# Performance work log

Measured on AMD Instinct MI355X. Metric: run time of the kernel, lower is better.

Reference implementation:

```python
import jax, jax.numpy as jnp
import numpy as np

B, S, H = 1, 4096, 2048
NH, NKV, HD = 8, 4, 256
I = 8192
EPS = 1e-6
THETA = 10000.0
WINDOW = 4096  # hardcoded sliding window for even layer_idx
LAYER_IDX = 0


def rms_norm(x, w):
    v = jnp.mean(jnp.square(x), axis=-1, keepdims=True)
    return x * jax.lax.rsqrt(v + EPS) * w


def rotate_half(x):
    h = x.shape[-1] // 2
    return jnp.concatenate([-x[..., h:], x[..., :h]], axis=-1)


def apply_rope(q, k, positions):
    # q: [B,S,NH,HD], k: [B,S,NKV,HD], positions: [B,S]
    inv_freq = 1.0 / (THETA ** (jnp.arange(0, HD, 2, dtype=jnp.float32) / HD))
    freqs = positions.astype(jnp.float32)[..., None] * inv_freq  # [B,S,HD/2]
    emb = jnp.concatenate([freqs, freqs], axis=-1)               # [B,S,HD]
    cos = jnp.cos(emb)[:, :, None, :]
    sin = jnp.sin(emb)[:, :, None, :]
    q = q * cos + rotate_half(q) * sin
    k = k * cos + rotate_half(k) * sin
    return q, k


def forward(hidden_states, q_w, k_w, v_w, o_w, gate_w, up_w, down_w, ln1_w, ln2_w,
            attention_mask, position_ids):
    # ---- input RMSNorm + attention ----
    residual = hidden_states
    x = rms_norm(hidden_states, ln1_w)

    q = (x @ q_w).reshape(B, S, NH, HD)
    k = (x @ k_w).reshape(B, S, NKV, HD)
    v = (x @ v_w).reshape(B, S, NKV, HD)
    q, k = apply_rope(q, k, position_ids)

    # GQA: repeat kv heads to match query heads
    groups = NH // NKV
    k = jnp.repeat(k, groups, axis=2)  # [B,S,NH,HD]
    v = jnp.repeat(v, groups, axis=2)

    # masks: padding mask AND causal AND (even layer) local window of WINDOW
    row = jnp.arange(S)[:, None]
    col = jnp.arange(S)[None, :]
    causal = col <= row                                   # [S,S]
    combined = causal[None, None] & (attention_mask[:, None, None, :] > 0)
    if LAYER_IDX % 2 == 0:
        keep = ~(col <= row - WINDOW)                     # mask out keys older than WINDOW
        combined = combined & keep[None, None]
    neg = jnp.finfo(jnp.float32).min
    bias = jnp.where(combined, 0.0, neg).astype(jnp.float32)  # [B,1,S,S]

    scale = HD ** -0.5
    scores = jnp.einsum('bqhd,bkhd->bhqk', q, k) * scale + bias
    probs = jax.nn.softmax(scores, axis=-1)
    attn = jnp.einsum('bhqk,bkhd->bqhd', probs, v).reshape(B, S, NH * HD)
    attn_out = attn @ o_w

    hidden_states = residual + attn_out

    # ---- post-attention RMSNorm + gated-GeLU MLP ----
    residual = hidden_states
    x = rms_norm(hidden_states, ln2_w)
    mlp = (jax.nn.gelu(x @ gate_w, approximate=True) * (x @ up_w)) @ down_w
    return residual + mlp


def setup_inputs() -> dict:
    key = jax.random.key(0)
    ks = jax.random.split(key, 9)
    std = 0.02
    n = lambda k, shp: jax.random.normal(k, shp, dtype=jnp.float32) * std
    return {
        'hidden_states': jax.random.normal(ks[0], (B, S, H), dtype=jnp.float32),
        'q_w': n(ks[1], (H, NH * HD)),
        'k_w': n(ks[2], (H, NKV * HD)),
        'v_w': n(ks[3], (H, NKV * HD)),
        'o_w': n(ks[4], (NH * HD, H)),
        'gate_w': n(ks[5], (H, I)),
        'up_w': n(ks[6], (H, I)),
        'down_w': n(ks[7], (I, H)),
        'ln1_w': jnp.ones((H,), jnp.float32),
        'ln2_w': jnp.ones((H,), jnp.float32),
        'attention_mask': jnp.ones((B, S), jnp.int32),
        'position_ids': jnp.broadcast_to(jnp.arange(S, dtype=jnp.int32)[None, :], (B, S)),
    }


def reference(hidden_states, q_w, k_w, v_w, o_w, gate_w, up_w, down_w, ln1_w, ln2_w,
              attention_mask, position_ids):
    return forward(hidden_states, q_w, k_w, v_w, o_w, gate_w, up_w, down_w,
                   ln1_w, ln2_w, attention_mask, position_ids)
```

## Files before the change

kernel.cpp:

```cpp
#include <hip/hip_runtime.h>
#include <hip/hip_bf16.h>
#include <math.h>

#define S_LEN 4096
#define HID   2048
#define NHEADS 8
#define NKVH   4
#define HDIM   256
#define FFN    8192
#define WIN    4096
#define QKV_LD 4096

typedef __bf16 bf16_t;
typedef __bf16 bf16x4 __attribute__((ext_vector_type(4)));
typedef __bf16 bf16x8 __attribute__((ext_vector_type(8)));
typedef float  floatx4 __attribute__((ext_vector_type(4)));

#define WAITCNT_VM0   0x0f70
#define WAITCNT_VM8   0x0f78
#define WAITCNT_LGKM0 0xc07f

__device__ inline float waveReduceSum(float v) {
#pragma unroll
    for (int o = 32; o > 0; o >>= 1) v += __shfl_xor(v, o);
    return v;
}
__device__ inline float blockReduceSum(float v, float* sh) {
    int tid = threadIdx.x;
    v = waveReduceSum(v);
    if ((tid & 63) == 0) sh[tid >> 6] = v;
    __syncthreads();
    v = sh[0] + sh[1] + sh[2] + sh[3];
    __syncthreads();
    return v;
}

template <typename T>
__global__ __launch_bounds__(256) void transpose_bf16_kernel(const T* __restrict__ in,
                                                             bf16_t* __restrict__ out,
                                                             int ldin, int ldout) {
    __shared__ float tile[32][33];
    int tx = threadIdx.x & 31;
    int ty = threadIdx.x >> 5;
    int c0 = blockIdx.x * 32;
    int r0 = blockIdx.y * 32;
#pragma unroll
    for (int i = 0; i < 4; ++i)
        tile[ty + i * 8][tx] = (float)in[(long long)(r0 + ty + i * 8) * ldin + c0 + tx];
    __syncthreads();
#pragma unroll
    for (int i = 0; i < 4; ++i)
        out[(long long)(c0 + ty + i * 8) * ldout + r0 + tx] = (bf16_t)tile[tx][ty + i * 8];
}

__global__ __launch_bounds__(256) void rmsnorm_kernel(const float* __restrict__ x,
                                                      const float* __restrict__ w,
                                                      bf16_t* __restrict__ out) {
    __shared__ float sh[4];
    int row = blockIdx.x;
    const float* xr = x + (long long)row * HID;
    float v[8];
    float ss = 0.f;
#pragma unroll
    for (int i = 0; i < 8; ++i) {
        v[i] = xr[threadIdx.x + i * 256];
        ss += v[i] * v[i];
    }
    ss = blockReduceSum(ss, sh);
    float sc = rsqrtf(ss * (1.0f / HID) + 1e-6f);
#pragma unroll
    for (int i = 0; i < 8; ++i) {
        int c = threadIdx.x + i * 256;
        out[(long long)row * HID + c] = (bf16_t)(v[i] * sc * w[c]);
    }
}

__global__ __launch_bounds__(256) void rope_kernel(bf16_t* __restrict__ qkv,
                                                   const int* __restrict__ pos_ids) {
    int s = blockIdx.x;
    float p = (float)pos_ids[s];
    for (int t = threadIdx.x; t < (NHEADS + NKVH) * (HDIM / 2); t += 256) {
        int head = t >> 7;
        int i = t & 127;
        float inv = expf(-(2.0f * (float)i / (float)HDIM) * 9.210340371976184f);
        float f = p * inv;
        float sn, cs;
        sincosf(f, &sn, &cs);
        int col = (head < NHEADS) ? head * HDIM : HID + (head - NHEADS) * HDIM;
        bf16_t* base = qkv + (long long)s * QKV_LD + col;
        float a = (float)base[i];
        float b = (float)base[i + 128];
        base[i]       = (bf16_t)(a * cs - b * sn);
        base[i + 128] = (bf16_t)(b * cs + a * sn);
    }
}

__global__ __launch_bounds__(256) void flash_attn_kernel(const bf16_t* __restrict__ qkv,
                                                         const bf16_t* __restrict__ vTg,
                                                         bf16_t* __restrict__ op0,
                                                         bf16_t* __restrict__ op1,
                                                         float* __restrict__ mlb,
                                                         const int* __restrict__ amask) {
    __shared__ bf16_t sK[64 * 256];
    __shared__ bf16_t sV[256 * 64];
    __shared__ bf16_t sPb[4 * 16 * 72];

    const int h = blockIdx.y;
    const int kh = blockIdx.z;
    const int tid = threadIdx.x;
    const int lane = tid & 63;
    const int w = tid >> 6;
    const int tl = lane & 15;
    const int quad = lane >> 4;

    const bf16_t* Qh = qkv + h * HDIM;
    const bf16_t* Kh = qkv + HID + (h >> 1) * HDIM;
    const bf16_t* Vh = vTg + (long long)(h >> 1) * HDIM * S_LEN;
    bf16_t* Op = kh ? op1 : op0;
    bf16_t* sP = sPb + w * (16 * 72);

#pragma unroll 1
    for (int half = 0; half < 2; ++half) {
        const int qi = half ? (63 - blockIdx.x) : blockIdx.x;
        const int qr0 = qi * 64;
        const int ntiles = qi + 1;
        const int mid = ntiles >> 1;
        const int t0 = kh ? mid : 0;
        const int t1 = kh ? ntiles : mid;
        const int irow = qr0 + w * 16 + tl;

        const bf16_t* qrow = Qh + (long long)irow * QKV_LD;
        bf16x8 qf[8];
#pragma unroll
        for (int ks = 0; ks < 8; ++ks)
            qf[ks] = *(const bf16x8*)(qrow + (ks * 4 + quad) * 8);

        floatx4 oacc[16] = {};
        float m_i = -3e38f, l_i = 0.f;

        bf16x8 stK[8], stV[8];
        auto load_tile = [&](int kt) {
#pragma unroll
            for (int it = 0; it < 8; ++it) {
                int s = it * 256 + tid;
                {
                    int m = s >> 5, sg = s & 31, g = sg ^ (m & 7);
                    stK[it] = *(const bf16x8*)(Kh + (long long)(kt + m) * QKV_LD + g * 8);
                }
                {
                    int m = s >> 3, sg = s & 7, g = sg ^ (m & 7);
                    stV[it] = *(const bf16x8*)(Vh + (long long)m * S_LEN + kt + g * 8);
                }
            }
        };

        if (t0 < t1) load_tile(t0 * 64);

#pragma unroll 1
        for (int t = t0; t < t1; ++t) {
            const int kt = t * 64;
#pragma unroll
            for (int it = 0; it < 8; ++it) {
                int s = it * 256 + tid;
                *(bf16x8*)(sK + s * 8) = stK[it];
                *(bf16x8*)(sV + s * 8) = stV[it];
            }
            __syncthreads();

            if (t + 1 < t1) load_tile((t + 1) * 64);
            __builtin_amdgcn_sched_barrier(0);

            floatx4 sacc[4] = {};
            __builtin_amdgcn_s_setprio(1);
#pragma unroll
            for (int ks = 0; ks < 8; ++ks) {
                bf16x8 kf[4];
#pragma unroll
                for (int ni = 0; ni < 4; ++ni) {
                    int row = ni * 16 + tl;
                    int ph = (ks * 4 + quad) ^ (row & 7);
                    kf[ni] = *(const bf16x8*)(sK + row * 256 + ph * 8);
                }
#pragma unroll
                for (int ni = 0; ni < 4; ++ni)
                    sacc[ni] = __builtin_amdgcn_mfma_f32_16x16x32_bf16(kf[ni], qf[ks], sacc[ni], 0, 0, 0);
            }
            __builtin_amdgcn_s_setprio(0);

            float sv[4][4];
            float mx = -3e38f;
#pragma unroll
            for (int ni = 0; ni < 4; ++ni) {
                int4 am = *(const int4*)(amask + kt + ni * 16 + quad * 4);
#pragma unroll
                for (int r = 0; r < 4; ++r) {
                    int j = kt + ni * 16 + quad * 4 + r;
                    int amr = (r == 0) ? am.x : (r == 1) ? am.y : (r == 2) ? am.z : am.w;
                    bool valid = (j <= irow) && (j > irow - WIN) && (amr > 0);
                    float x = valid ? sacc[ni][r] * 0.0625f : -3e38f;
                    sv[ni][r] = x;
                    mx = fmaxf(mx, x);
                }
            }
            mx = fmaxf(mx, __shfl_xor(mx, 16));
            mx = fmaxf(mx, __shfl_xor(mx, 32));
            bool noresc = __all(mx <= m_i + 8.0f);
            float mnew = noresc ? m_i : fmaxf(m_i, mx);
            float rs = 0.f;
#pragma unroll
            for (int ni = 0; ni < 4; ++ni) {
                bf16x4 pk;
#pragma unroll
                for (int r = 0; r < 4; ++r) {
                    float p = (sv[ni][r] > -1e37f) ? __expf(sv[ni][r] - mnew) : 0.f;
                    rs += p;
                    pk[r] = (bf16_t)p;
                }
                *(bf16x4*)(sP + tl * 72 + ni * 16 + quad * 4) = pk;
            }
            rs += __shfl_xor(rs, 16);
            rs += __shfl_xor(rs, 32);
            if (noresc) {
                l_i += rs;
            } else {
                float alpha = __expf(m_i - mnew);
                l_i = l_i * alpha + rs;
                m_i = mnew;
                floatx4 av;
#pragma unroll
                for (int r = 0; r < 4; ++r) av[r] = __shfl(alpha, quad * 4 + r);
#pragma unroll
                for (int dt = 0; dt < 16; ++dt) oacc[dt] *= av;
            }

            __builtin_amdgcn_s_setprio(1);
#pragma unroll
            for (int k2 = 0; k2 < 2; ++k2) {
                bf16x8 pf = *(const bf16x8*)(sP + tl * 72 + k2 * 32 + quad * 8);
#pragma unroll
                for (int dt = 0; dt < 16; ++dt) {
                    int d = dt * 16 + tl;
                    int ph = (k2 * 4 + quad) ^ (d & 7);
                    bf16x8 vf = *(const bf16x8*)(sV + d * 64 + ph * 8);
                    oacc[dt] = __builtin_amdgcn_mfma_f32_16x16x32_bf16(pf, vf, oacc[dt], 0, 0, 0);
                }
            }
            __builtin_amdgcn_s_setprio(0);
            __syncthreads();
        }

        floatx4 inv;
#pragma unroll
        for (int r = 0; r < 4; ++r) {
            float lv = __shfl(l_i, quad * 4 + r);
            inv[r] = (lv > 0.f) ? 1.0f / lv : 0.f;
        }
#pragma unroll
        for (int dt = 0; dt < 16; ++dt) {
#pragma unroll
            for (int r = 0; r < 4; ++r) {
                long long row = qr0 + w * 16 + quad * 4 + r;
                Op[row * HID + h * HDIM + dt * 16 + tl] = (bf16_t)(oacc[dt][r] * inv[r]);
            }
        }
        if (quad == 0) {
            long long mi = ((long long)(kh * NHEADS + h) * S_LEN + qr0 + w * 16 + tl) * 2;
            mlb[mi] = m_i;
            mlb[mi + 1] = l_i;
        }
    }
}

__global__ __launch_bounds__(256) void combine_kernel(bf16_t* __restrict__ op0,
                                                      const bf16_t* __restrict__ op1,
                                                      const float* __restrict__ mlb) {
    int h = blockIdx.x;
    int row = blockIdx.y;
    int d = threadIdx.x;
    long long m0i = ((long long)h * S_LEN + row) * 2;
    long long m1i = ((long long)(NHEADS + h) * S_LEN + row) * 2;
    float m0 = mlb[m0i], l0 = mlb[m0i + 1];
    float m1 = mlb[m1i], l1 = mlb[m1i + 1];
    float M = fmaxf(m0, m1);
    float w0 = (l0 > 0.f) ? l0 * __expf(m0 - M) : 0.f;
    float w1 = (l1 > 0.f) ? l1 * __expf(m1 - M) : 0.f;
    float inv = 1.0f / (w0 + w1);
    long long idx = (long long)row * HID + h * HDIM + d;
    float v = (w0 * (float)op0[idx] + w1 * (float)op1[idx]) * inv;
    op0[idx] = (bf16_t)v;
}

template <int MODE>
__global__ __launch_bounds__(256) void gemm_kernel(const bf16_t* __restrict__ A, int lda,
                                                   const bf16_t* __restrict__ Bt, int ldb,
                                                   void* __restrict__ Cv, int ldc,
                                                   const void* __restrict__ aux, int K) {
    __shared__ bf16_t smem[2][2 * 128 * 64];

    const int tid = threadIdx.x;
    const int n0 = blockIdx.x * 128;
    const int m0 = blockIdx.y * 128;

    const int lane = tid & 63;
    const int wid = tid >> 6;
    const int wm = (wid >> 1) * 64;
    const int wn = (wid & 1) * 64;
    const int tl = lane & 15;
    const int quad = lane >> 4;

    floatx4 acc[4][4] = {};

    auto stage = [&](int buf, int k0) {
        bf16_t* sA = smem[buf];
        bf16_t* sB = smem[buf] + 128 * 64;
#pragma unroll
        for (int it = 0; it < 4; ++it) {
            int s = it * 256 + tid;
            int m = s >> 3;
            int sg = s & 7;
            int g = sg ^ (m & 7);
            const bf16_t* ga = A + (long long)(m0 + m) * lda + k0 + g * 8;
            __builtin_amdgcn_global_load_lds((const __attribute__((address_space(1))) void*)ga,
                                             (__attribute__((address_space(3))) void*)(sA + s * 8),
                                             16, 0, 0);
            const bf16_t* gb = Bt + (long long)(n0 + m) * ldb + k0 + g * 8;
            __builtin_amdgcn_global_load_lds((const __attribute__((address_space(1))) void*)gb,
                                             (__attribute__((address_space(3))) void*)(sB + s * 8),
                                             16, 0, 0);
        }
    };

    stage(0, 0);
    int cur = 0;

    for (int k0 = 0; k0 < K; k0 += 64) {
        if (k0 + 64 < K) {
            stage(cur ^ 1, k0 + 64);
            __builtin_amdgcn_s_waitcnt(WAITCNT_VM8);
        } else {
            __builtin_amdgcn_s_waitcnt(WAITCNT_VM0);
        }
        __builtin_amdgcn_s_barrier();
        __builtin_amdgcn_sched_barrier(0);

        const bf16_t* sA = smem[cur];
        const bf16_t* sB = smem[cur] + 128 * 64;
#pragma unroll
        for (int kk = 0; kk < 2; ++kk) {
            bf16x8 af[4], bfr[4];
#pragma unroll
            for (int mi = 0; mi < 4; ++mi) {
                int m = wm + mi * 16 + tl;
                int sg = (kk * 4 + quad) ^ (m & 7);
                af[mi] = *(const bf16x8*)(sA + m * 64 + sg * 8);
            }
#pragma unroll
            for (int ni = 0; ni < 4; ++ni) {
                int n = wn + ni * 16 + tl;
                int sg = (kk * 4 + quad) ^ (n & 7);
                bfr[ni] = *(const bf16x8*)(sB + n * 64 + sg * 8);
            }
#pragma unroll
            for (int mi = 0; mi < 4; ++mi)
#pragma unroll
                for (int ni = 0; ni < 4; ++ni)
                    acc[mi][ni] = __builtin_amdgcn_mfma_f32_16x16x32_bf16(af[mi], bfr[ni], acc[mi][ni], 0, 0, 0);
        }

        __builtin_amdgcn_s_waitcnt(WAITCNT_LGKM0);
        __builtin_amdgcn_sched_barrier(0);
        __builtin_amdgcn_s_barrier();
        cur ^= 1;
    }

#pragma unroll
    for (int mi = 0; mi < 4; ++mi) {
#pragma unroll
        for (int ni = 0; ni < 4; ++ni) {
#pragma unroll
            for (int r = 0; r < 4; ++r) {
                int gr = m0 + wm + mi * 16 + quad * 4 + r;
                int gc = n0 + wn + ni * 16 + tl;
                long long idx = (long long)gr * ldc + gc;
                float v = acc[mi][ni][r];
                if (MODE == 0) {
                    ((bf16_t*)Cv)[idx] = (bf16_t)v;
                } else if (MODE == 1) {
                    ((float*)Cv)[idx] = ((const float*)aux)[idx] + v;
                } else {
                    float g = (float)((const bf16_t*)aux)[idx];
                    float t = 0.7978845608028654f * (g + 0.044715f * g * g * g);
                    float ge = 0.5f * g * (1.0f + tanhf(t));
                    ((bf16_t*)Cv)[idx] = (bf16_t)(ge * v);
                }
            }
        }
    }
}

extern "C" void kernel_launch(void* const* d_in, const int* in_sizes, int n_in,
                              void* d_out, int out_size, void* d_ws, size_t ws_size,
                              hipStream_t stream) {
    const float* hidden = (const float*)d_in[0];
    const float* q_w    = (const float*)d_in[1];
    const float* k_w    = (const float*)d_in[2];
    const float* v_w    = (const float*)d_in[3];
    const float* o_w    = (const float*)d_in[4];
    const float* gate_w = (const float*)d_in[5];
    const float* up_w   = (const float*)d_in[6];
    const float* down_w = (const float*)d_in[7];
    const float* ln1_w  = (const float*)d_in[8];
    const float* ln2_w  = (const float*)d_in[9];
    const int* amask    = (const int*)d_in[10];
    const int* pos_ids  = (const int*)d_in[11];
    float* out = (float*)d_out;

    const size_t MB = 1ull << 20;
    char* ws = (char*)d_ws;
    bf16_t* wqT = (bf16_t*)(ws + 0 * MB);
    bf16_t* wkT = (bf16_t*)(ws + 8 * MB);
    bf16_t* wvT = (bf16_t*)(ws + 12 * MB);
    bf16_t* woT = (bf16_t*)(ws + 16 * MB);
    bf16_t* wgT = (bf16_t*)(ws + 24 * MB);
    bf16_t* wuT = (bf16_t*)(ws + 56 * MB);
    bf16_t* wdT = (bf16_t*)(ws + 88 * MB);
    bf16_t* xb    = (bf16_t*)(ws + 120 * MB);
    bf16_t* qkvb  = (bf16_t*)(ws + 136 * MB);
    bf16_t* vT    = (bf16_t*)(ws + 168 * MB);
    bf16_t* op0   = (bf16_t*)(ws + 120 * MB);
    bf16_t* op1   = (bf16_t*)(ws + 176 * MB);
    float*  mlb   = (float*) (ws + 192 * MB);
    bf16_t* attnb = (bf16_t*)(ws + 120 * MB);
    bf16_t* xb2   = (bf16_t*)(ws + 120 * MB);
    bf16_t* gateb = (bf16_t*)(ws + 136 * MB);
    (void)ws_size; (void)in_sizes; (void)n_in; (void)out_size;

    dim3 blk(256);

    transpose_bf16_kernel<float><<<dim3(64, 64), blk, 0, stream>>>(q_w, wqT, 2048, 2048);
    transpose_bf16_kernel<float><<<dim3(32, 64), blk, 0, stream>>>(k_w, wkT, 1024, 2048);
    transpose_bf16_kernel<float><<<dim3(32, 64), blk, 0, stream>>>(v_w, wvT, 1024, 2048);
    transpose_bf16_kernel<float><<<dim3(64, 64), blk, 0, stream>>>(o_w, woT, 2048, 2048);
    transpose_bf16_kernel<float><<<dim3(256, 64), blk, 0, stream>>>(gate_w, wgT, 8192, 2048);
    transpose_bf16_kernel<float><<<dim3(256, 64), blk, 0, stream>>>(up_w, wuT, 8192, 2048);
    transpose_bf16_kernel<float><<<dim3(64, 256), blk, 0, stream>>>(down_w, wdT, 2048, 8192);

    rmsnorm_kernel<<<dim3(S_LEN), blk, 0, stream>>>(hidden, ln1_w, xb);

    gemm_kernel<0><<<dim3(32, 32), blk, 0, stream>>>(xb, HID, wqT, HID, qkvb, QKV_LD, nullptr, HID);

    rope_kernel<<<dim3(S_LEN), blk, 0, stream>>>(qkvb, pos_ids);

    transpose_bf16_kernel<bf16_t><<<dim3(32, 128), blk, 0, stream>>>(qkvb + 3072, vT, QKV_LD, S_LEN);

    flash_attn_kernel<<<dim3(32, NHEADS, 2), blk, 0, stream>>>(qkvb, vT, op0, op1, mlb, amask);
    combine_kernel<<<dim3(NHEADS, S_LEN), blk, 0, stream>>>(op0, op1, mlb);

    gemm_kernel<1><<<dim3(16, 32), blk, 0, stream>>>(attnb, 2048, woT, 2048, out, 2048, hidden, 2048);

    rmsnorm_kernel<<<dim3(S_LEN), blk, 0, stream>>>(out, ln2_w, xb2);

    gemm_kernel<0><<<dim3(64, 32), blk, 0, stream>>>(xb2, HID, wgT, HID, gateb, FFN, nullptr, HID);
    gemm_kernel<2><<<dim3(64, 32), blk, 0, stream>>>(xb2, HID, wuT, HID, gateb, FFN, gateb, HID);
    gemm_kernel<1><<<dim3(16, 32), blk, 0, stream>>>(gateb, FFN, wdT, FFN, out, 2048, out, FFN);
}
```

Baseline: 1.152 ms.

## Split attention KV range four ways with 32-key tiles and higher occupancy

```diff
diff --git a/kernel.cpp b/kernel.cpp
--- a/kernel.cpp
+++ b/kernel.cpp
@@ -10,6 +10,7 @@
 #define FFN    8192
 #define WIN    4096
 #define QKV_LD 4096
+#define KVBLK  32
 
 typedef __bf16 bf16_t;
 typedef __bf16 bf16x4 __attribute__((ext_vector_type(4)));
@@ -95,15 +96,17 @@
     }
 }
 
-__global__ __launch_bounds__(256) void flash_attn_kernel(const bf16_t* __restrict__ qkv,
-                                                         const bf16_t* __restrict__ vTg,
-                                                         bf16_t* __restrict__ op0,
-                                                         bf16_t* __restrict__ op1,
-                                                         float* __restrict__ mlb,
-                                                         const int* __restrict__ amask) {
-    __shared__ bf16_t sK[64 * 256];
-    __shared__ bf16_t sV[256 * 64];
-    __shared__ bf16_t sPb[4 * 16 * 72];
+__global__ __launch_bounds__(256, 3) void flash_attn_kernel(const bf16_t* __restrict__ qkv,
+                                                            const bf16_t* __restrict__ vTg,
+                                                            bf16_t* __restrict__ op0,
+                                                            bf16_t* __restrict__ op1,
+                                                            bf16_t* __restrict__ op2,
+                                                            bf16_t* __restrict__ op3,
+                                                            float* __restrict__ mlb,
+                                                            const int* __restrict__ amask) {
+    __shared__ bf16_t sK[KVBLK * 256];
+    __shared__ bf16_t sV[256 * KVBLK];
+    __shared__ bf16_t sPb[4 * 16 * 40];
 
     const int h = blockIdx.y;
     const int kh = blockIdx.z;
@@ -116,17 +119,18 @@
     const bf16_t* Qh = qkv + h * HDIM;
     const bf16_t* Kh = qkv + HID + (h >> 1) * HDIM;
     const bf16_t* Vh = vTg + (long long)(h >> 1) * HDIM * S_LEN;
-    bf16_t* Op = kh ? op1 : op0;
-    bf16_t* sP = sPb + w * (16 * 72);
+    bf16_t* Op = (kh == 0) ? op0 : (kh == 1) ? op1 : (kh == 2) ? op2 : op3;
+    bf16_t* sP = sPb + w * (16 * 40);
 
 #pragma unroll 1
     for (int half = 0; half < 2; ++half) {
         const int qi = half ? (63 - blockIdx.x) : blockIdx.x;
         const int qr0 = qi * 64;
-        const int ntiles = qi + 1;
-        const int mid = ntiles >> 1;
-        const int t0 = kh ? mid : 0;
-        const int t1 = kh ? ntiles : mid;
+        const int ntiles = 2 * qi + 2;
+        const int q4 = ntiles >> 2;
+        const int r4 = ntiles & 3;
+        const int t0 = kh * q4 + ((kh < r4) ? kh : r4);
+        const int t1 = t0 + q4 + ((kh < r4) ? 1 : 0);
         const int irow = qr0 + w * 16 + tl;
 
         const bf16_t* qrow = Qh + (long long)irow * QKV_LD;
@@ -138,59 +142,59 @@
         floatx4 oacc[16] = {};
         float m_i = -3e38f, l_i = 0.f;
 
-        bf16x8 stK[8], stV[8];
+        bf16x8 stK[4], stV[4];
         auto load_tile = [&](int kt) {
 #pragma unroll
-            for (int it = 0; it < 8; ++it) {
+            for (int it = 0; it < 4; ++it) {
                 int s = it * 256 + tid;
                 {
                     int m = s >> 5, sg = s & 31, g = sg ^ (m & 7);
                     stK[it] = *(const bf16x8*)(Kh + (long long)(kt + m) * QKV_LD + g * 8);
                 }
                 {
-                    int m = s >> 3, sg = s & 7, g = sg ^ (m & 7);
+                    int m = s >> 2, sg = s & 3, g = sg ^ (m & 3);
                     stV[it] = *(const bf16x8*)(Vh + (long long)m * S_LEN + kt + g * 8);
                 }
             }
         };
 
-        if (t0 < t1) load_tile(t0 * 64);
+        if (t0 < t1) load_tile(t0 * KVBLK);
 
 #pragma unroll 1
         for (int t = t0; t < t1; ++t) {
-            const int kt = t * 64;
-#pragma unroll
-            for (int it = 0; it < 8; ++it) {
+            const int kt = t * KVBLK;
+#pragma unroll
+            for (int it = 0; it < 4; ++it) {
                 int s = it * 256 + tid;
                 *(bf16x8*)(sK + s * 8) = stK[it];
                 *(bf16x8*)(sV + s * 8) = stV[it];
             }
             __syncthreads();
 
-            if (t + 1 < t1) load_tile((t + 1) * 64);
+            if (t + 1 < t1) load_tile((t + 1) * KVBLK);
             __builtin_amdgcn_sched_barrier(0);
 
-            floatx4 sacc[4] = {};
+            floatx4 sacc[2] = {};
             __builtin_amdgcn_s_setprio(1);
 #pragma unroll
             for (int ks = 0; ks < 8; ++ks) {
-                bf16x8 kf[4];
-#pragma unroll
-                for (int ni = 0; ni < 4; ++ni) {
+                bf16x8 kf[2];
+#pragma unroll
+                for (int ni = 0; ni < 2; ++ni) {
                     int row = ni * 16 + tl;
                     int ph = (ks * 4 + quad) ^ (row & 7);
                     kf[ni] = *(const bf16x8*)(sK + row * 256 + ph * 8);
                 }
 #pragma unroll
-                for (int ni = 0; ni < 4; ++ni)
+                for (int ni = 0; ni < 2; ++ni)
                     sacc[ni] = __builtin_amdgcn_mfma_f32_16x16x32_bf16(kf[ni], qf[ks], sacc[ni], 0, 0, 0);
             }
             __builtin_amdgcn_s_setprio(0);
 
-            float sv[4][4];
+            float sv[2][4];
             float mx = -3e38f;
 #pragma unroll
-            for (int ni = 0; ni < 4; ++ni) {
+            for (int ni = 0; ni < 2; ++ni) {
                 int4 am = *(const int4*)(amask + kt + ni * 16 + quad * 4);
 #pragma unroll
                 for (int r = 0; r < 4; ++r) {
@@ -208,7 +212,7 @@
             float mnew = noresc ? m_i : fmaxf(m_i, mx);
             float rs = 0.f;
 #pragma unroll
-            for (int ni = 0; ni < 4; ++ni) {
+            for (int ni = 0; ni < 2; ++ni) {
                 bf16x4 pk;
 #pragma unroll
                 for (int r = 0; r < 4; ++r) {
@@ -216,7 +220,7 @@
                     rs += p;
                     pk[r] = (bf16_t)p;
                 }
-                *(bf16x4*)(sP + tl * 72 + ni * 16 + quad * 4) = pk;
+                *(bf16x4*)(sP + tl * 40 + ni * 16 + quad * 4) = pk;
             }
             rs += __shfl_xor(rs, 16);
             rs += __shfl_xor(rs, 32);
@@ -234,14 +238,13 @@
             }
 
             __builtin_amdgcn_s_setprio(1);
-#pragma unroll
-            for (int k2 = 0; k2 < 2; ++k2) {
-                bf16x8 pf = *(const bf16x8*)(sP + tl * 72 + k2 * 32 + quad * 8);
+            {
+                bf16x8 pf = *(const bf16x8*)(sP + tl * 40 + quad * 8);
 #pragma unroll
                 for (int dt = 0; dt < 16; ++dt) {
                     int d = dt * 16 + tl;
-                    int ph = (k2 * 4 + quad) ^ (d & 7);
-                    bf16x8 vf = *(const bf16x8*)(sV + d * 64 + ph * 8);
+                    int ph = quad ^ (d & 3);
+                    bf16x8 vf = *(const bf16x8*)(sV + d * KVBLK + ph * 8);
                     oacc[dt] = __builtin_amdgcn_mfma_f32_16x16x32_bf16(pf, vf, oacc[dt], 0, 0, 0);
                 }
             }
@@ -273,20 +276,31 @@
 
 __global__ __launch_bounds__(256) void combine_kernel(bf16_t* __restrict__ op0,
                                                       const bf16_t* __restrict__ op1,
+                                                      const bf16_t* __restrict__ op2,
+                                                      const bf16_t* __restrict__ op3,
                                                       const float* __restrict__ mlb) {
     int h = blockIdx.x;
     int row = blockIdx.y;
     int d = threadIdx.x;
-    long long m0i = ((long long)h * S_LEN + row) * 2;
-    long long m1i = ((long long)(NHEADS + h) * S_LEN + row) * 2;
-    float m0 = mlb[m0i], l0 = mlb[m0i + 1];
-    float m1 = mlb[m1i], l1 = mlb[m1i + 1];
-    float M = fmaxf(m0, m1);
-    float w0 = (l0 > 0.f) ? l0 * __expf(m0 - M) : 0.f;
-    float w1 = (l1 > 0.f) ? l1 * __expf(m1 - M) : 0.f;
-    float inv = 1.0f / (w0 + w1);
+    float m[4], l[4];
+#pragma unroll
+    for (int k = 0; k < 4; ++k) {
+        long long mi = ((long long)(k * NHEADS + h) * S_LEN + row) * 2;
+        m[k] = mlb[mi];
+        l[k] = mlb[mi + 1];
+    }
+    float M = fmaxf(fmaxf(m[0], m[1]), fmaxf(m[2], m[3]));
+    float wk[4];
+    float wsum = 0.f;
+#pragma unroll
+    for (int k = 0; k < 4; ++k) {
+        wk[k] = (l[k] > 0.f) ? l[k] * __expf(m[k] - M) : 0.f;
+        wsum += wk[k];
+    }
+    float inv = 1.0f / wsum;
     long long idx = (long long)row * HID + h * HDIM + d;
-    float v = (w0 * (float)op0[idx] + w1 * (float)op1[idx]) * inv;
+    float v = (wk[0] * (float)op0[idx] + wk[1] * (float)op1[idx] +
+               wk[2] * (float)op2[idx] + wk[3] * (float)op3[idx]) * inv;
     op0[idx] = (bf16_t)v;
 }
 
@@ -429,6 +443,8 @@
     bf16_t* vT    = (bf16_t*)(ws + 168 * MB);
     bf16_t* op0   = (bf16_t*)(ws + 120 * MB);
     bf16_t* op1   = (bf16_t*)(ws + 176 * MB);
+    bf16_t* op2   = (bf16_t*)d_out;
+    bf16_t* op3   = (bf16_t*)d_out + (16 * MB / sizeof(bf16_t));
     float*  mlb   = (float*) (ws + 192 * MB);
     bf16_t* attnb = (bf16_t*)(ws + 120 * MB);
     bf16_t* xb2   = (bf16_t*)(ws + 120 * MB);
@@ -453,8 +469,8 @@
 
     transpose_bf16_kernel<bf16_t><<<dim3(32, 128), blk, 0, stream>>>(qkvb + 3072, vT, QKV_LD, S_LEN);
 
-    flash_attn_kernel<<<dim3(32, NHEADS, 2), blk, 0, stream>>>(qkvb, vT, op0, op1, mlb, amask);
-    combine_kernel<<<dim3(NHEADS, S_LEN), blk, 0, stream>>>(op0, op1, mlb);
+    flash_attn_kernel<<<dim3(32, NHEADS, 4), blk, 0, stream>>>(qkvb, vT, op0, op1, op2, op3, mlb, amask);
+    combine_kernel<<<dim3(NHEADS, S_LEN), blk, 0, stream>>>(op0, op1, op2, op3, mlb);
 
     gemm_kernel<1><<<dim3(16, 32), blk, 0, stream>>>(attnb, 2048, woT, 2048, out, 2048, hidden, 2048);
 
```

New measurement: 1.306 ms. 13.4% more time.

## Replace 128x128 GEMM with 512-thread 256x256/128x256 tiled kernel with interleaved fragment loads

Applied to the files above, without the earlier changes.

```diff
diff --git a/kernel.cpp b/kernel.cpp
--- a/kernel.cpp
+++ b/kernel.cpp
@@ -290,39 +290,44 @@
     op0[idx] = (bf16_t)v;
 }
 
-template <int MODE>
-__global__ __launch_bounds__(256) void gemm_kernel(const bf16_t* __restrict__ A, int lda,
-                                                   const bf16_t* __restrict__ Bt, int ldb,
-                                                   void* __restrict__ Cv, int ldc,
-                                                   const void* __restrict__ aux, int K) {
-    __shared__ bf16_t smem[2][2 * 128 * 64];
+template <int BM, int MODE>
+__global__ __launch_bounds__(512) void gemm256_kernel(const bf16_t* __restrict__ A, int lda,
+                                                      const bf16_t* __restrict__ Bt, int ldb,
+                                                      void* __restrict__ Cv, int ldc,
+                                                      const void* __restrict__ aux, int K) {
+    constexpr int LPT = BM / 64 + 4;
+    constexpr int WAIT_VM_LPT = 0x0f70 | LPT;
+    constexpr int MF = BM / 32;
+    __shared__ bf16_t smem[2][(BM + 256) * 64];
 
     const int tid = threadIdx.x;
-    const int n0 = blockIdx.x * 128;
-    const int m0 = blockIdx.y * 128;
-
+    const int n0 = blockIdx.x * 256;
+    const int m0 = blockIdx.y * BM;
     const int lane = tid & 63;
     const int wid = tid >> 6;
-    const int wm = (wid >> 1) * 64;
-    const int wn = (wid & 1) * 64;
+    const int wm = (wid >> 2) * (BM / 2);
+    const int wn = (wid & 3) * 64;
     const int tl = lane & 15;
     const int quad = lane >> 4;
 
-    floatx4 acc[4][4] = {};
+    floatx4 acc[MF][4] = {};
 
     auto stage = [&](int buf, int k0) {
         bf16_t* sA = smem[buf];
-        bf16_t* sB = smem[buf] + 128 * 64;
-#pragma unroll
-        for (int it = 0; it < 4; ++it) {
-            int s = it * 256 + tid;
-            int m = s >> 3;
-            int sg = s & 7;
-            int g = sg ^ (m & 7);
+        bf16_t* sB = smem[buf] + BM * 64;
+#pragma unroll
+        for (int it = 0; it < BM / 64; ++it) {
+            int s = it * 512 + tid;
+            int m = s >> 3, sg = s & 7, g = sg ^ (m & 7);
             const bf16_t* ga = A + (long long)(m0 + m) * lda + k0 + g * 8;
             __builtin_amdgcn_global_load_lds((const __attribute__((address_space(1))) void*)ga,
                                              (__attribute__((address_space(3))) void*)(sA + s * 8),
                                              16, 0, 0);
+        }
+#pragma unroll
+        for (int it = 0; it < 4; ++it) {
+            int s = it * 512 + tid;
+            int m = s >> 3, sg = s & 7, g = sg ^ (m & 7);
             const bf16_t* gb = Bt + (long long)(n0 + m) * ldb + k0 + g * 8;
             __builtin_amdgcn_global_load_lds((const __attribute__((address_space(1))) void*)gb,
                                              (__attribute__((address_space(3))) void*)(sB + s * 8),
@@ -330,13 +335,14 @@
         }
     };
 
+    const int nk = K >> 6;
     stage(0, 0);
     int cur = 0;
 
-    for (int k0 = 0; k0 < K; k0 += 64) {
-        if (k0 + 64 < K) {
-            stage(cur ^ 1, k0 + 64);
-            __builtin_amdgcn_s_waitcnt(WAITCNT_VM8);
+    for (int t = 0; t < nk; ++t) {
+        if (t + 1 < nk) {
+            stage(cur ^ 1, (t + 1) * 64);
+            __builtin_amdgcn_s_waitcnt(WAIT_VM_LPT);
         } else {
             __builtin_amdgcn_s_waitcnt(WAITCNT_VM0);
         }
@@ -344,27 +350,115 @@
         __builtin_amdgcn_sched_barrier(0);
 
         const bf16_t* sA = smem[cur];
-        const bf16_t* sB = smem[cur] + 128 * 64;
-#pragma unroll
-        for (int kk = 0; kk < 2; ++kk) {
-            bf16x8 af[4], bfr[4];
+        const bf16_t* sB = smem[cur] + BM * 64;
+
+        if constexpr (BM == 256) {
+            bf16x8 a[4][2], b0[2][2], b1[2][2];
 #pragma unroll
             for (int mi = 0; mi < 4; ++mi) {
                 int m = wm + mi * 16 + tl;
-                int sg = (kk * 4 + quad) ^ (m & 7);
-                af[mi] = *(const bf16x8*)(sA + m * 64 + sg * 8);
-            }
-#pragma unroll
-            for (int ni = 0; ni < 4; ++ni) {
+#pragma unroll
+                for (int kk = 0; kk < 2; ++kk) {
+                    int sg = (kk * 4 + quad) ^ (m & 7);
+                    a[mi][kk] = *(const bf16x8*)(sA + m * 64 + sg * 8);
+                }
+            }
+#pragma unroll
+            for (int ni = 0; ni < 2; ++ni) {
                 int n = wn + ni * 16 + tl;
-                int sg = (kk * 4 + quad) ^ (n & 7);
-                bfr[ni] = *(const bf16x8*)(sB + n * 64 + sg * 8);
-            }
+#pragma unroll
+                for (int kk = 0; kk < 2; ++kk) {
+                    int sg = (kk * 4 + quad) ^ (n & 7);
+                    b0[ni][kk] = *(const bf16x8*)(sB + n * 64 + sg * 8);
+                }
+            }
+            __builtin_amdgcn_s_setprio(1);
 #pragma unroll
             for (int mi = 0; mi < 4; ++mi)
 #pragma unroll
-                for (int ni = 0; ni < 4; ++ni)
-                    acc[mi][ni] = __builtin_amdgcn_mfma_f32_16x16x32_bf16(af[mi], bfr[ni], acc[mi][ni], 0, 0, 0);
+                for (int ni = 0; ni < 2; ++ni)
+#pragma unroll
+                    for (int kk = 0; kk < 2; ++kk)
+                        acc[mi][ni] = __builtin_amdgcn_mfma_f32_16x16x32_bf16(a[mi][kk], b0[ni][kk], acc[mi][ni], 0, 0, 0);
+            __builtin_amdgcn_s_setprio(0);
+            __builtin_amdgcn_sched_barrier(0);
+#pragma unroll
+            for (int ni = 0; ni < 2; ++ni) {
+                int n = wn + 32 + ni * 16 + tl;
+#pragma unroll
+                for (int kk = 0; kk < 2; ++kk) {
+                    int sg = (kk * 4 + quad) ^ (n & 7);
+                    b1[ni][kk] = *(const bf16x8*)(sB + n * 64 + sg * 8);
+                }
+            }
+            __builtin_amdgcn_s_setprio(1);
+#pragma unroll
+            for (int mi = 0; mi < 4; ++mi)
+#pragma unroll
+                for (int ni = 0; ni < 2; ++ni)
+#pragma unroll
+                    for (int kk = 0; kk < 2; ++kk)
+                        acc[mi][2 + ni] = __builtin_amdgcn_mfma_f32_16x16x32_bf16(a[mi][kk], b1[ni][kk], acc[mi][2 + ni], 0, 0, 0);
+            __builtin_amdgcn_s_setprio(0);
+            __builtin_amdgcn_sched_barrier(0);
+#pragma unroll
+            for (int mi = 0; mi < 4; ++mi) {
+                int m = wm + 64 + mi * 16 + tl;
+#pragma unroll
+                for (int kk = 0; kk < 2; ++kk) {
+                    int sg = (kk * 4 + quad) ^ (m & 7);
+                    a[mi][kk] = *(const bf16x8*)(sA + m * 64 + sg * 8);
+                }
+            }
+            __builtin_amdgcn_s_setprio(1);
+#pragma unroll
+            for (int mi = 0; mi < 4; ++mi)
+#pragma unroll
+                for (int ni = 0; ni < 2; ++ni)
+#pragma unroll
+                    for (int kk = 0; kk < 2; ++kk)
+                        acc[4 + mi][2 + ni] = __builtin_amdgcn_mfma_f32_16x16x32_bf16(a[mi][kk], b1[ni][kk], acc[4 + mi][2 + ni], 0, 0, 0);
+            __builtin_amdgcn_s_setprio(0);
+            __builtin_amdgcn_sched_barrier(0);
+            __builtin_amdgcn_s_setprio(1);
+#pragma unroll
+            for (int mi = 0; mi < 4; ++mi)
+#pragma unroll
+                for (int ni = 0; ni < 2; ++ni)
+#pragma unroll
+                    for (int kk = 0; kk < 2; ++kk)
+                        acc[4 + mi][ni] = __builtin_amdgcn_mfma_f32_16x16x32_bf16(a[mi][kk], b0[ni][kk], acc[4 + mi][ni], 0, 0, 0);
+            __builtin_amdgcn_s_setprio(0);
+        } else {
+            bf16x8 a[4][2];
+#pragma unroll
+            for (int mi = 0; mi < 4; ++mi) {
+                int m = wm + mi * 16 + tl;
+#pragma unroll
+                for (int kk = 0; kk < 2; ++kk) {
+                    int sg = (kk * 4 + quad) ^ (m & 7);
+                    a[mi][kk] = *(const bf16x8*)(sA + m * 64 + sg * 8);
+                }
+            }
+            __builtin_amdgcn_sched_barrier(0);
+#pragma unroll
+            for (int nh = 0; nh < 4; ++nh) {
+                bf16x8 b[2];
+                int n = wn + nh * 16 + tl;
+#pragma unroll
+                for (int kk = 0; kk < 2; ++kk) {
+                    int sg = (kk * 4 + quad) ^ (n & 7);
+                    b[kk] = *(const bf16x8*)(sB + n * 64 + sg * 8);
+                }
+                __builtin_amdgcn_s_setprio(1);
+#pragma unroll
+                for (int mi = 0; mi < 4; ++mi)
+#pragma unroll
+                    for (int kk = 0; kk < 2; ++kk)
+                        acc[mi][nh] = __builtin_amdgcn_mfma_f32_16x16x32_bf16(a[mi][kk], b[kk], acc[mi][nh], 0, 0, 0);
+                __builtin_amdgcn_s_setprio(0);
+                __builtin_amdgcn_sched_barrier(0);
+            }
         }
 
         __builtin_amdgcn_s_waitcnt(WAITCNT_LGKM0);
@@ -374,15 +468,16 @@
     }
 
 #pragma unroll
-    for (int mi = 0; mi < 4; ++mi) {
-#pragma unroll
-        for (int ni = 0; ni < 4; ++ni) {
+    for (int f = 0; f < MF; ++f) {
+        int moff = (BM == 256) ? ((f >> 2) * 64 + (f & 3) * 16) : (f * 16);
+#pragma unroll
+        for (int j = 0; j < 4; ++j) {
 #pragma unroll
             for (int r = 0; r < 4; ++r) {
-                int gr = m0 + wm + mi * 16 + quad * 4 + r;
-                int gc = n0 + wn + ni * 16 + tl;
+                int gr = m0 + wm + moff + quad * 4 + r;
+                int gc = n0 + wn + j * 16 + tl;
                 long long idx = (long long)gr * ldc + gc;
-                float v = acc[mi][ni][r];
+                float v = acc[f][j][r];
                 if (MODE == 0) {
                     ((bf16_t*)Cv)[idx] = (bf16_t)v;
                 } else if (MODE == 1) {
@@ -436,6 +531,7 @@
     (void)ws_size; (void)in_sizes; (void)n_in; (void)out_size;
 
     dim3 blk(256);
+    dim3 blkG(512);
 
     transpose_bf16_kernel<float><<<dim3(64, 64), blk, 0, stream>>>(q_w, wqT, 2048, 2048);
     transpose_bf16_kernel<float><<<dim3(32, 64), blk, 0, stream>>>(k_w, wkT, 1024, 2048);
@@ -447,7 +543,7 @@
 
     rmsnorm_kernel<<<dim3(S_LEN), blk, 0, stream>>>(hidden, ln1_w, xb);
 
-    gemm_kernel<0><<<dim3(32, 32), blk, 0, stream>>>(xb, HID, wqT, HID, qkvb, QKV_LD, nullptr, HID);
+    gemm256_kernel<256, 0><<<dim3(16, 16), blkG, 0, stream>>>(xb, HID, wqT, HID, qkvb, QKV_LD, nullptr, HID);
 
     rope_kernel<<<dim3(S_LEN), blk, 0, stream>>>(qkvb, pos_ids);
 
@@ -456,11 +552,11 @@
     flash_attn_kernel<<<dim3(32, NHEADS, 2), blk, 0, stream>>>(qkvb, vT, op0, op1, mlb, amask);
     combine_kernel<<<dim3(NHEADS, S_LEN), blk, 0, stream>>>(op0, op1, mlb);
 
-    gemm_kernel<1><<<dim3(16, 32), blk, 0, stream>>>(attnb, 2048, woT, 2048, out, 2048, hidden, 2048);
+    gemm256_kernel<128, 1><<<dim3(8, 32), blkG, 0, stream>>>(attnb, 2048, woT, 2048, out, 2048, hidden, 2048);
 
     rmsnorm_kernel<<<dim3(S_LEN), blk, 0, stream>>>(out, ln2_w, xb2);
 
-    gemm_kernel<0><<<dim3(64, 32), blk, 0, stream>>>(xb2, HID, wgT, HID, gateb, FFN, nullptr, HID);
-    gemm_kernel<2><<<dim3(64, 32), blk, 0, stream>>>(xb2, HID, wuT, HID, gateb, FFN, gateb, HID);
-    gemm_kernel<1><<<dim3(16, 32), blk, 0, stream>>>(gateb, FFN, wdT, FFN, out, 2048, out, FFN);
-}
+    gemm256_kernel<256, 0><<<dim3(32, 16), blkG, 0, stream>>>(xb2, HID, wgT, HID, gateb, FFN, nullptr, HID);
+    gemm256_kernel<256, 2><<<dim3(32, 16), blkG, 0, stream>>>(xb2, HID, wuT, HID, gateb, FFN, gateb, HID);
+    gemm256_kernel<128, 1><<<dim3(8, 32), blkG, 0, stream>>>(gateb, FFN, wdT, FFN, out, 2048, out, FFN);
+}
```

New measurement: 1.135 ms. No clear change (-1.4%).
